# Kernel optimization log

Hardware: AMD Instinct MI355X
Metric: run time of the kernel (lower is better)

## Reference

```python
import jax, jax.numpy as jnp
import numpy as np

N_GENS, D, N_REL, L = 32, 256, 512, 6


def setup_inputs() -> dict:
    key = jax.random.key(0)
    k1, k2, k3 = jax.random.split(key, 3)
    # scale by 1/sqrt(D) so length-6 chain products stay O(1) numerically
    gen_reps = jax.random.normal(k1, (N_GENS, D, D), dtype=jnp.float32) / jnp.sqrt(jnp.float32(D))
    r1_idx = jax.random.randint(k2, (N_REL, L), 0, N_GENS, dtype=jnp.int32)
    r2_idx = jax.random.randint(k3, (N_REL, L), 0, N_GENS, dtype=jnp.int32)
    return {"gen_reps": gen_reps, "r1_idx": r1_idx, "r2_idx": r2_idx}


def _chain_product(gen_reps, idx):
    # idx: [n_rel, L] -> batched chain product prod_i gen_reps[idx[:, i]], shape [n_rel, D, D]
    init = gen_reps[idx[:, 0]]  # [n_rel, D, D]

    def step(carry, ids):
        return jnp.einsum('rij,rjk->rik', carry, gen_reps[ids]), None

    out, _ = jax.lax.scan(step, init, idx[:, 1:].T)  # scan over chain positions 1..L-1
    return out


def reference(gen_reps, r1_idx, r2_idx):
    A = _chain_product(gen_reps, r1_idx)  # [n_rel, D, D]
    B = _chain_product(gen_reps, r2_idx)  # [n_rel, D, D]
    diff = A - B
    dists = jnp.sqrt(jnp.sum(diff * diff, axis=(-2, -1)))  # Frobenius norm per relation
    return jnp.mean(dists)
```

## Files before the change

### kernel.cpp

```cpp
#include <hip/hip_runtime.h>
#include <hip/hip_bf16.h>


#define NREL 512

typedef __attribute__((ext_vector_type(8))) short bf16x8;
typedef __attribute__((ext_vector_type(4))) float f32x4;

static __device__ __forceinline__ float ubits(unsigned u)
{
    union { unsigned u; float f; } v; v.u = u; return v.f;
}
static __device__ __forceinline__ unsigned f2bu(float f)
{
    union { __hip_bfloat16 h; unsigned short s; } v;
    v.h = __float2bfloat16(f);
    return (unsigned)v.s;
}

__global__ void prep_kernel(const float* __restrict__ G,
                            __hip_bfloat16* __restrict__ Gbf,
                            __hip_bfloat16* __restrict__ Gt,
                            float* __restrict__ part)
{
    int idx = blockIdx.x * 256 + threadIdx.x;
    int g   = idx >> 16;
    int rem = idx & 65535;
    int i   = rem >> 8;
    int j   = rem & 255;
    __hip_bfloat16 h = __float2bfloat16(G[idx]);
    Gbf[idx] = h;
    Gt[(g << 16) + (j << 8) + i] = h;
    if (idx < NREL) part[idx] = 0.0f;
}

__device__ __forceinline__ int m_off(int row, int col)
{
    return ((row << 9) + (col << 1)) ^ ((row & 7) << 4);
}

static __device__ __forceinline__
void stageChunk(const __hip_bfloat16* __restrict__ gm, int jc, char* dstbuf,
                int tid, int wave)
{
    const int sr0 = tid >> 5, ss = tid & 31;
#pragma unroll
    for (int i = 0; i < 2; ++i) {
        int sr = i * 16 + sr0;
        int ks = (ss - 2 * sr) & 31;
        const __hip_bfloat16* src = gm + jc * 8192 + sr * 256 + ks * 8;
        char* dst = dstbuf + i * 8192 + wave * 1024;
        __builtin_amdgcn_global_load_lds(
            (const __attribute__((address_space(1))) void*)src,
            (__attribute__((address_space(3))) void*)dst, 16, 0, 0);
    }
}

template<int MODE>
static __device__ __forceinline__
void substep(const __hip_bfloat16* __restrict__ gt, char* __restrict__ Gs,
             char* __restrict__ myM,
             bf16x8 (&cur)[8], unsigned (&AF)[32], float& dsq,
             int tid, int wave, int lr, int lg)
{
#pragma unroll
    for (int jc = 0; jc < 8; ++jc) {
        stageChunk(gt, jc, Gs, tid, wave);
        __syncthreads();
#pragma unroll
        for (int jl = 0; jl < 2; ++jl) {
            const int cl = jl * 16 + lr;
            f32x4 acc = {0.f, 0.f, 0.f, 0.f};
#pragma unroll
            for (int kk = 0; kk < 8; ++kk) {
                int slot = (4 * kk + lg + 2 * cl) & 31;
                bf16x8 b = *(const bf16x8*)(Gs + cl * 512 + slot * 16);
                acc = __builtin_amdgcn_mfma_f32_16x16x32_bf16(cur[kk], b, acc, 0, 0, 0);
            }
            if (MODE == 0) {
                const int colb = jc * 32 + cl;
#pragma unroll
                for (int q = 0; q < 4; ++q)
                    *(unsigned short*)(myM + m_off(lg * 4 + q, colb)) =
                        (unsigned short)f2bu(acc[q]);
            } else if (MODE == 1) {
                AF[(jc * 2 + jl) * 2 + 0] = f2bu(acc[0]) | (f2bu(acc[1]) << 16);
                AF[(jc * 2 + jl) * 2 + 1] = f2bu(acc[2]) | (f2bu(acc[3]) << 16);
            } else {
                unsigned w0 = AF[(jc * 2 + jl) * 2 + 0];
                unsigned w1 = AF[(jc * 2 + jl) * 2 + 1];
                float d0 = acc[0] - ubits(w0 << 16);
                float d1 = acc[1] - ubits(w0 & 0xffff0000u);
                float d2 = acc[2] - ubits(w1 << 16);
                float d3 = acc[3] - ubits(w1 & 0xffff0000u);
                dsq += d0 * d0 + d1 * d1 + d2 * d2 + d3 * d3;
            }
        }
        __syncthreads();
    }
    if (MODE == 0) {
#pragma unroll
        for (int kk = 0; kk < 8; ++kk)
            cur[kk] = *(const bf16x8*)(myM + m_off(lr, kk * 32 + lg * 8));
    }
}

__global__ __launch_bounds__(512, 4)
void chain_kernel(const __hip_bfloat16* __restrict__ Gbf,
                  const __hip_bfloat16* __restrict__ Gt,
                  const int* __restrict__ r1,
                  const int* __restrict__ r2,
                  float* __restrict__ part)
{
    __shared__ __align__(16) char Gs[16384];
    __shared__ __align__(16) char M[8][8192];

    const int tid  = threadIdx.x;
    const int wave = tid >> 6;
    const int lane = tid & 63;
    const int lr   = lane & 15;
    const int lg   = lane >> 4;
    const int r    = blockIdx.x >> 1;
    const int h    = blockIdx.x & 1;
    const int wrow = h * 128 + wave * 16;

    const int* iA = r1 + r * 6;
    const int* iB = r2 + r * 6;

    char* myM = M[wave];
    bf16x8   cur[8];
    unsigned AF[32];
    float    dsq = 0.f;

    {
        const __hip_bfloat16* g0 = Gbf + (iA[0] << 16);
#pragma unroll
        for (int kk = 0; kk < 8; ++kk)
            cur[kk] = *(const bf16x8*)(g0 + ((wrow + lr) << 8) + kk * 32 + lg * 8);
    }
#pragma unroll 1
    for (int t = 1; t <= 4; ++t)
        substep<0>(Gt + (iA[t] << 16), Gs, myM, cur, AF, dsq, tid, wave, lr, lg);
    substep<1>(Gt + (iA[5] << 16), Gs, myM, cur, AF, dsq, tid, wave, lr, lg);

    {
        const __hip_bfloat16* g0 = Gbf + (iB[0] << 16);
#pragma unroll
        for (int kk = 0; kk < 8; ++kk)
            cur[kk] = *(const bf16x8*)(g0 + ((wrow + lr) << 8) + kk * 32 + lg * 8);
    }
#pragma unroll 1
    for (int t = 1; t <= 4; ++t)
        substep<0>(Gt + (iB[t] << 16), Gs, myM, cur, AF, dsq, tid, wave, lr, lg);
    substep<2>(Gt + (iB[5] << 16), Gs, myM, cur, AF, dsq, tid, wave, lr, lg);

#pragma unroll
    for (int off = 32; off > 0; off >>= 1)
        dsq += __shfl_down(dsq, off);
    __syncthreads();
    float* red = (float*)Gs;
    if (lane == 0) red[wave] = dsq;
    __syncthreads();
    if (tid == 0) {
        float s = 0.f;
#pragma unroll
        for (int w = 0; w < 8; ++w) s += red[w];
        atomicAdd(part + r, s);
    }
}

__global__ void finish_kernel(const float* __restrict__ part, float* __restrict__ out)
{
    int lane = threadIdx.x;
    float v = 0.f;
#pragma unroll
    for (int i = 0; i < 8; ++i)
        v += sqrtf(part[lane + i * 64]);
#pragma unroll
    for (int off = 32; off > 0; off >>= 1)
        v += __shfl_down(v, off);
    if (lane == 0) out[0] = v * (1.0f / 512.0f);
}

extern "C" void kernel_launch(void* const* d_in, const int* in_sizes, int n_in,
                              void* d_out, int out_size, void* d_ws, size_t ws_size,
                              hipStream_t stream)
{
    const float* G   = (const float*)d_in[0];
    const int*   r1  = (const int*)d_in[1];
    const int*   r2  = (const int*)d_in[2];
    float*       out = (float*)d_out;

    char* ws = (char*)d_ws;
    __hip_bfloat16* Gbf  = (__hip_bfloat16*)ws;
    __hip_bfloat16* Gt   = (__hip_bfloat16*)(ws + (4u << 20));
    float*          part = (float*)(ws + (8u << 20));

    prep_kernel<<<8192, 256, 0, stream>>>(G, Gbf, Gt, part);
    chain_kernel<<<1024, 512, 0, stream>>>(Gbf, Gt, r1, r2, part);
    finish_kernel<<<1, 64, 0, stream>>>(part, out);
}
```

Before: 323.3 us.

## Process full relation per block with two row tiles and double-buffered LDS staging

Each block now handles a whole relation (32 rows per wave, two MFMA accumulators sharing each B fragment) instead of splitting a relation across two blocks. This halves the redundant staging of each generator matrix into LDS and removes the atomic. The G chunk staging is double-buffered so the next chunk (including the first chunk of the next chain step) loads while the current one is multiplied, dropping one barrier per chunk. In exchange, LDS use grows to about 160KB per block, occupancy drops to one block per CU, and the grid shrinks to 512 blocks.

Measured after the change: 283.9 us. 1.14x faster.

```diff
diff --git a/kernel.cpp b/kernel.cpp
--- a/kernel.cpp
+++ b/kernel.cpp
@@ -58,114 +58,144 @@
 
 template<int MODE>
 static __device__ __forceinline__
-void substep(const __hip_bfloat16* __restrict__ gt, char* __restrict__ Gs,
-             char* __restrict__ myM,
-             bf16x8 (&cur)[8], unsigned (&AF)[32], float& dsq,
+void substep(const __hip_bfloat16* __restrict__ gt,
+             const __hip_bfloat16* __restrict__ gnext,
+             char* __restrict__ GsB, char* __restrict__ myM,
+             bf16x8 (&cur)[2][8], unsigned (&AF)[2][32], float& dsq,
              int tid, int wave, int lr, int lg)
 {
 #pragma unroll
     for (int jc = 0; jc < 8; ++jc) {
-        stageChunk(gt, jc, Gs, tid, wave);
-        __syncthreads();
+        const int buf = jc & 1;
+        if (jc < 7)      stageChunk(gt,    jc + 1, GsB + (buf ^ 1) * 16384, tid, wave);
+        else if (gnext)  stageChunk(gnext, 0,      GsB + (buf ^ 1) * 16384, tid, wave);
+
+        const char* gs = GsB + buf * 16384;
 #pragma unroll
         for (int jl = 0; jl < 2; ++jl) {
             const int cl = jl * 16 + lr;
-            f32x4 acc = {0.f, 0.f, 0.f, 0.f};
+            f32x4 acc0 = {0.f, 0.f, 0.f, 0.f};
+            f32x4 acc1 = {0.f, 0.f, 0.f, 0.f};
 #pragma unroll
             for (int kk = 0; kk < 8; ++kk) {
                 int slot = (4 * kk + lg + 2 * cl) & 31;
-                bf16x8 b = *(const bf16x8*)(Gs + cl * 512 + slot * 16);
-                acc = __builtin_amdgcn_mfma_f32_16x16x32_bf16(cur[kk], b, acc, 0, 0, 0);
+                bf16x8 b = *(const bf16x8*)(gs + cl * 512 + slot * 16);
+                acc0 = __builtin_amdgcn_mfma_f32_16x16x32_bf16(cur[0][kk], b, acc0, 0, 0, 0);
+                acc1 = __builtin_amdgcn_mfma_f32_16x16x32_bf16(cur[1][kk], b, acc1, 0, 0, 0);
             }
             if (MODE == 0) {
                 const int colb = jc * 32 + cl;
 #pragma unroll
-                for (int q = 0; q < 4; ++q)
+                for (int q = 0; q < 4; ++q) {
                     *(unsigned short*)(myM + m_off(lg * 4 + q, colb)) =
-                        (unsigned short)f2bu(acc[q]);
+                        (unsigned short)f2bu(acc0[q]);
+                    *(unsigned short*)(myM + m_off(16 + lg * 4 + q, colb)) =
+                        (unsigned short)f2bu(acc1[q]);
+                }
             } else if (MODE == 1) {
-                AF[(jc * 2 + jl) * 2 + 0] = f2bu(acc[0]) | (f2bu(acc[1]) << 16);
-                AF[(jc * 2 + jl) * 2 + 1] = f2bu(acc[2]) | (f2bu(acc[3]) << 16);
+                const int jt = (jc * 2 + jl) * 2;
+                AF[0][jt]     = f2bu(acc0[0]) | (f2bu(acc0[1]) << 16);
+                AF[0][jt + 1] = f2bu(acc0[2]) | (f2bu(acc0[3]) << 16);
+                AF[1][jt]     = f2bu(acc1[0]) | (f2bu(acc1[1]) << 16);
+                AF[1][jt + 1] = f2bu(acc1[2]) | (f2bu(acc1[3]) << 16);
             } else {
-                unsigned w0 = AF[(jc * 2 + jl) * 2 + 0];
-                unsigned w1 = AF[(jc * 2 + jl) * 2 + 1];
-                float d0 = acc[0] - ubits(w0 << 16);
-                float d1 = acc[1] - ubits(w0 & 0xffff0000u);
-                float d2 = acc[2] - ubits(w1 << 16);
-                float d3 = acc[3] - ubits(w1 & 0xffff0000u);
-                dsq += d0 * d0 + d1 * d1 + d2 * d2 + d3 * d3;
+                const int jt = (jc * 2 + jl) * 2;
+                unsigned a0 = AF[0][jt], a1 = AF[0][jt + 1];
+                unsigned b0 = AF[1][jt], b1 = AF[1][jt + 1];
+                float d0 = acc0[0] - ubits(a0 << 16);
+                float d1 = acc0[1] - ubits(a0 & 0xffff0000u);
+                float d2 = acc0[2] - ubits(a1 << 16);
+                float d3 = acc0[3] - ubits(a1 & 0xffff0000u);
+                float e0 = acc1[0] - ubits(b0 << 16);
+                float e1 = acc1[1] - ubits(b0 & 0xffff0000u);
+                float e2 = acc1[2] - ubits(b1 << 16);
+                float e3 = acc1[3] - ubits(b1 & 0xffff0000u);
+                dsq += d0*d0 + d1*d1 + d2*d2 + d3*d3;
+                dsq += e0*e0 + e1*e1 + e2*e2 + e3*e3;
             }
         }
         __syncthreads();
     }
     if (MODE == 0) {
 #pragma unroll
-        for (int kk = 0; kk < 8; ++kk)
-            cur[kk] = *(const bf16x8*)(myM + m_off(lr, kk * 32 + lg * 8));
-    }
-}
-
-__global__ __launch_bounds__(512, 4)
+        for (int rt = 0; rt < 2; ++rt)
+#pragma unroll
+            for (int kk = 0; kk < 8; ++kk)
+                cur[rt][kk] = *(const bf16x8*)(myM + m_off(rt * 16 + lr, kk * 32 + lg * 8));
+    }
+}
+
+__global__ __launch_bounds__(512, 1)
 void chain_kernel(const __hip_bfloat16* __restrict__ Gbf,
                   const __hip_bfloat16* __restrict__ Gt,
                   const int* __restrict__ r1,
                   const int* __restrict__ r2,
                   float* __restrict__ part)
 {
-    __shared__ __align__(16) char Gs[16384];
-    __shared__ __align__(16) char M[8][8192];
+    __shared__ __align__(16) char Gs[2][16384];
+    __shared__ __align__(16) char M[8][16384];
 
     const int tid  = threadIdx.x;
     const int wave = tid >> 6;
     const int lane = tid & 63;
     const int lr   = lane & 15;
     const int lg   = lane >> 4;
-    const int r    = blockIdx.x >> 1;
-    const int h    = blockIdx.x & 1;
-    const int wrow = h * 128 + wave * 16;
+    const int r    = blockIdx.x;
+    const int wrow = wave * 32;
 
     const int* iA = r1 + r * 6;
     const int* iB = r2 + r * 6;
 
+    char* GsB = (char*)Gs;
     char* myM = M[wave];
-    bf16x8   cur[8];
-    unsigned AF[32];
+    bf16x8   cur[2][8];
+    unsigned AF[2][32];
     float    dsq = 0.f;
 
     {
         const __hip_bfloat16* g0 = Gbf + (iA[0] << 16);
 #pragma unroll
-        for (int kk = 0; kk < 8; ++kk)
-            cur[kk] = *(const bf16x8*)(g0 + ((wrow + lr) << 8) + kk * 32 + lg * 8);
-    }
+        for (int rt = 0; rt < 2; ++rt)
+#pragma unroll
+            for (int kk = 0; kk < 8; ++kk)
+                cur[rt][kk] = *(const bf16x8*)(g0 + ((wrow + rt * 16 + lr) << 8) + kk * 32 + lg * 8);
+    }
+    stageChunk(Gt + (iA[1] << 16), 0, GsB, tid, wave);
+    __syncthreads();
 #pragma unroll 1
     for (int t = 1; t <= 4; ++t)
-        substep<0>(Gt + (iA[t] << 16), Gs, myM, cur, AF, dsq, tid, wave, lr, lg);
-    substep<1>(Gt + (iA[5] << 16), Gs, myM, cur, AF, dsq, tid, wave, lr, lg);
+        substep<0>(Gt + (iA[t] << 16), Gt + (iA[t + 1] << 16), GsB, myM,
+                   cur, AF, dsq, tid, wave, lr, lg);
+    substep<1>(Gt + (iA[5] << 16), Gt + (iB[1] << 16), GsB, myM,
+               cur, AF, dsq, tid, wave, lr, lg);
 
     {
         const __hip_bfloat16* g0 = Gbf + (iB[0] << 16);
 #pragma unroll
-        for (int kk = 0; kk < 8; ++kk)
-            cur[kk] = *(const bf16x8*)(g0 + ((wrow + lr) << 8) + kk * 32 + lg * 8);
+        for (int rt = 0; rt < 2; ++rt)
+#pragma unroll
+            for (int kk = 0; kk < 8; ++kk)
+                cur[rt][kk] = *(const bf16x8*)(g0 + ((wrow + rt * 16 + lr) << 8) + kk * 32 + lg * 8);
     }
 #pragma unroll 1
     for (int t = 1; t <= 4; ++t)
-        substep<0>(Gt + (iB[t] << 16), Gs, myM, cur, AF, dsq, tid, wave, lr, lg);
-    substep<2>(Gt + (iB[5] << 16), Gs, myM, cur, AF, dsq, tid, wave, lr, lg);
+        substep<0>(Gt + (iB[t] << 16), Gt + (iB[t + 1] << 16), GsB, myM,
+                   cur, AF, dsq, tid, wave, lr, lg);
+    substep<2>(Gt + (iB[5] << 16), nullptr, GsB, myM,
+               cur, AF, dsq, tid, wave, lr, lg);
 
 #pragma unroll
     for (int off = 32; off > 0; off >>= 1)
         dsq += __shfl_down(dsq, off);
     __syncthreads();
-    float* red = (float*)Gs;
+    float* red = (float*)GsB;
     if (lane == 0) red[wave] = dsq;
     __syncthreads();
     if (tid == 0) {
         float s = 0.f;
 #pragma unroll
         for (int w = 0; w < 8; ++w) s += red[w];
-        atomicAdd(part + r, s);
+        part[r] = s;
     }
 }
 
@@ -197,6 +227,6 @@
     float*          part = (float*)(ws + (8u << 20));
 
     prep_kernel<<<8192, 256, 0, stream>>>(G, Gbf, Gt, part);
-    chain_kernel<<<1024, 512, 0, stream>>>(Gbf, Gt, r1, r2, part);
+    chain_kernel<<<NREL, 512, 0, stream>>>(Gbf, Gt, r1, r2, part);
     finish_kernel<<<1, 64, 0, stream>>>(part, out);
 }
```
